# Kernel tuning notes

Measured on AMD Instinct MI355X. Metric: run time of the kernel, lower is better.

Reference implementation:

```python
import jax, jax.numpy as jnp
import numpy as np

B, S, E, H = 8, 2048, 1024, 4
D = E // H  # per-head attention embed_dim (torch MHA with num_heads=1)


def setup_inputs() -> dict:
    key = jax.random.key(0)
    ks = jax.random.split(key, 7)
    scale = 0.02
    return {
        "x": jax.random.normal(ks[0], (B, S, E), dtype=jnp.float32),
        # outer linear: torch Linear(E, E) -> y = x @ W.T + b
        "W_lin": jax.random.normal(ks[1], (E, E), dtype=jnp.float32) * scale,
        "b_lin": jnp.zeros((E,), dtype=jnp.float32),
        # per-head MultiheadAttention params, stacked over H heads
        # in_proj: [3D, D] weight, [3D] bias per head (q,k,v stacked)
        "W_in": jax.random.normal(ks[2], (H, 3 * D, D), dtype=jnp.float32) * scale,
        "b_in": jnp.zeros((H, 3 * D), dtype=jnp.float32),
        # out_proj: [D, D] weight, [D] bias per head
        "W_out": jax.random.normal(ks[3], (H, D, D), dtype=jnp.float32) * scale,
        "b_out": jnp.zeros((H, D), dtype=jnp.float32),
    }


def _forward(x, W_lin, b_lin, W_in, b_in, W_out, b_out):
    # outer projection
    x_proj = jnp.einsum("bse,fe->bsf", x, W_lin) + b_lin          # [B,S,E]
    # torch.chunk(dim=-1) into H contiguous slices of width D == reshape
    xs = x_proj.reshape(B, S, H, D)                                 # [B,S,H,D]
    # per-head in_proj (q,k,v share input; weights stacked as [3D, D])
    qkv = jnp.einsum("bshd,hed->bshe", xs, W_in) + b_in             # [B,S,H,3D]
    q, k, v = jnp.split(qkv, 3, axis=-1)                            # each [B,S,H,D]
    # scaled dot-product attention per head (inner num_heads=1 -> head dim D)
    scores = jnp.einsum("bshd,bthd->bhst", q, k) / jnp.sqrt(jnp.float32(D))
    attn = jax.nn.softmax(scores, axis=-1)                          # [B,H,S,S]
    out = jnp.einsum("bhst,bthd->bshd", attn, v)                    # [B,S,H,D]
    # per-head out_proj
    out = jnp.einsum("bshd,hed->bshe", out, W_out) + b_out          # [B,S,H,D]
    # concat heads back along feature dim
    return out.reshape(B, S, E)


def reference(x, W_lin, b_lin, W_in, b_in, W_out, b_out):
    return _forward(x, W_lin, b_lin, W_in, b_in, W_out, b_out)
```

## Files before the change

kernel.cpp:

```cpp
#include <hip/hip_runtime.h>


typedef unsigned short u16;
typedef short s8v __attribute__((ext_vector_type(8)));
typedef float f4v __attribute__((ext_vector_type(4)));
typedef unsigned short us8v __attribute__((ext_vector_type(8)));

typedef const __attribute__((address_space(1))) void* gas_t;
typedef __attribute__((address_space(3))) void* las_t;

#define QSCALE 0.09016844f

__device__ __forceinline__ u16 f2bf(float f) {
  unsigned u = __builtin_bit_cast(unsigned, f);
  unsigned r = u + 0x7FFFu + ((u >> 16) & 1u);
  return (u16)(r >> 16);
}

__device__ __forceinline__ unsigned cvtpk(float a, float b) {
  unsigned r;
  asm("v_cvt_pk_bf16_f32 %0, %1, %2" : "=v"(r) : "v"(a), "v"(b));
  return r;
}

__device__ __forceinline__ void gload16(const void* g, void* l) {
  __builtin_amdgcn_global_load_lds((gas_t)g, (las_t)l, 16, 0, 0);
}

__global__ void cast_kernel(const float* __restrict__ in, u16* __restrict__ out, int n4) {
  int i = blockIdx.x * blockDim.x + threadIdx.x;
  const int stride = gridDim.x * blockDim.x;
  for (; i < n4; i += stride) {
    const float4 v = reinterpret_cast<const float4*>(in)[i];
    ushort4 o;
    o.x = f2bf(v.x); o.y = f2bf(v.y); o.z = f2bf(v.z); o.w = f2bf(v.w);
    reinterpret_cast<ushort4*>(out)[i] = o;
  }
}

__global__ void cast_weights(const float* __restrict__ Wl, const float* __restrict__ Wi,
                             const float* __restrict__ Wo,
                             u16* __restrict__ WLb, u16* __restrict__ WIb,
                             u16* __restrict__ WOb) {
  const int i = blockIdx.x * blockDim.x + threadIdx.x;
  const float* src;
  u16* dst;
  int j;
  float sc = 1.0f;
  if (i < 262144) {
    src = Wl; dst = WLb; j = i;
  } else if (i < 458752) {
    src = Wi; dst = WIb; j = i - 262144;
    if (((j >> 6) % 768) < 256) sc = QSCALE;
  } else {
    src = Wo; dst = WOb; j = i - 458752;
  }
  const float4 v = reinterpret_cast<const float4*>(src)[j];
  ushort4 o;
  o.x = f2bf(v.x * sc); o.y = f2bf(v.y * sc); o.z = f2bf(v.z * sc); o.w = f2bf(v.w * sc);
  reinterpret_cast<ushort4*>(dst)[j] = o;
}

template <int MODE>
__global__ void __launch_bounds__(256, 2) gemm128(
    const u16* __restrict__ A, const u16* __restrict__ Bw,
    const float* __restrict__ bias,
    u16* __restrict__ outB, float* __restrict__ outF,
    u16* __restrict__ Qo, u16* __restrict__ Ko, u16* __restrict__ Vo)
{
  constexpr int K    = (MODE == 0) ? 1024 : 256;
  constexpr int LDA  = 1024;
  constexpr int LDB  = (MODE == 0) ? 1024 : 256;
  constexpr int SMEM = (MODE == 1) ? 35072 : 32768;

  const int bx = blockIdx.x, ny = blockIdx.y, h = blockIdx.z;
  const int tid = threadIdx.x;
  const int wid = tid >> 6, l = tid & 63;
  const int l15 = l & 15, lg = l >> 4;
  const int wr = wid >> 1, wc = wid & 1;

  __shared__ __align__(16) char smem[SMEM];
  char* Al = smem;
  char* Bl = smem + 16384;

  const u16* Abase = A + (size_t)bx * 128 * LDA + ((MODE == 0) ? 0 : h * 256);
  const size_t bwoff = (MODE == 0) ? 0
                      : ((MODE == 1) ? (size_t)h * 768 * 256 : (size_t)h * 256 * 256);
  const u16* Bbase = Bw + bwoff + (size_t)ny * 128 * LDB;

  f4v acc[4][4];
#pragma unroll
  for (int i = 0; i < 4; ++i)
#pragma unroll
    for (int j = 0; j < 4; ++j) acc[i][j] = f4v{0.f, 0.f, 0.f, 0.f};

  for (int k0 = 0; k0 < K; k0 += 64) {
    __syncthreads();
#pragma unroll
    for (int ii = 0; ii < 4; ++ii) {
      const int i = wid * 4 + ii;
      const int row = i * 8 + (l >> 3);
      const int c = l & 7;
      gload16(Abase + (size_t)row * LDA + k0 + ((c ^ (row & 7)) << 3), Al + i * 1024);
    }
#pragma unroll
    for (int ii = 0; ii < 4; ++ii) {
      const int i = wid * 4 + ii;
      const int row = i * 8 + (l >> 3);
      const int c = l & 7;
      gload16(Bbase + (size_t)row * LDB + k0 + ((c ^ (row & 7)) << 3), Bl + i * 1024);
    }
    __syncthreads();
#pragma unroll
    for (int kf = 0; kf < 2; ++kf) {
      s8v a[4];
#pragma unroll
      for (int mf = 0; mf < 4; ++mf) {
        const int row = wr * 64 + mf * 16 + l15;
        a[mf] = *reinterpret_cast<const s8v*>(
            Al + row * 128 + (((kf * 32 + lg * 8) << 1) ^ ((row & 7) << 4)));
      }
#pragma unroll
      for (int nf = 0; nf < 4; ++nf) {
        const int n = wc * 64 + nf * 16 + l15;
        const s8v b = *reinterpret_cast<const s8v*>(
            Bl + n * 128 + (((kf * 32 + lg * 8) << 1) ^ ((n & 7) << 4)));
#pragma unroll
        for (int mf = 0; mf < 4; ++mf)
          acc[mf][nf] = __builtin_amdgcn_mfma_f32_16x16x32_bf16(a[mf], b, acc[mf][nf], 0, 0, 0);
      }
    }
  }

  const int mbase = bx * 128 + wr * 64;
  const int nbase = ny * 128 + wc * 64;

  if constexpr (MODE == 0) {
#pragma unroll
    for (int nf = 0; nf < 4; ++nf) {
      const int colg = nbase + nf * 16 + l15;
      const float bv = bias[colg];
#pragma unroll
      for (int mf = 0; mf < 4; ++mf)
#pragma unroll
        for (int r = 0; r < 4; ++r) {
          const int mr = mbase + mf * 16 + lg * 4 + r;
          outB[(size_t)mr * 1024 + colg] = f2bf(acc[mf][nf][r] + bv);
        }
    }
  } else if constexpr (MODE == 2) {
#pragma unroll
    for (int nf = 0; nf < 4; ++nf) {
      const int colg = nbase + nf * 16 + l15;
      const float bv = bias[h * 256 + colg];
#pragma unroll
      for (int mf = 0; mf < 4; ++mf)
#pragma unroll
        for (int r = 0; r < 4; ++r) {
          const int mr = mbase + mf * 16 + lg * 4 + r;
          outF[(size_t)mr * 1024 + h * 256 + colg] = acc[mf][nf][r] + bv;
        }
    }
  } else {
    if (ny < 4) {
      u16* dst = (ny < 2) ? Qo : Ko;
      const int cb = (ny < 2) ? 0 : 256;
#pragma unroll
      for (int nf = 0; nf < 4; ++nf) {
        const int colg = nbase + nf * 16 + l15;
        const float bscale = (ny < 2) ? QSCALE : 1.0f;
        const float bv = bias[h * 768 + colg] * bscale;
        const int d = colg - cb;
#pragma unroll
        for (int mf = 0; mf < 4; ++mf)
#pragma unroll
          for (int r = 0; r < 4; ++r) {
            const int mr = mbase + mf * 16 + lg * 4 + r;
            const int b = mr >> 11, s = mr & 2047;
            dst[((size_t)(b * 4 + h) * 2048 + s) * 256 + d] = f2bf(acc[mf][nf][r] + bv);
          }
      }
    } else {
      __syncthreads();
      short* tr = reinterpret_cast<short*>(smem);
#pragma unroll
      for (int nf = 0; nf < 4; ++nf) {
        const int colg = nbase + nf * 16 + l15;
        const float bv = bias[h * 768 + colg];
        const int cl = wc * 64 + nf * 16 + l15;
#pragma unroll
        for (int mf = 0; mf < 4; ++mf)
#pragma unroll
          for (int r = 0; r < 4; ++r) {
            const int rl = wr * 64 + mf * 16 + lg * 4 + r;
            tr[rl * 137 + cl] = (short)f2bf(acc[mf][nf][r] + bv);
          }
      }
      __syncthreads();
      const int b = bx >> 4;
#pragma unroll
      for (int rep = 0; rep < 8; ++rep) {
        const int u = rep * 256 + tid;
        const int d = u >> 4, sb = u & 15;
        const int dglob = (ny - 4) * 128 + d;
        const int tile = (bx & 15) * 2 + (sb >> 3);
        const int c = sb & 7;
        const int kA = 32 * (c >> 2) + 8 * ((2 * c) & 3) + 4 * ((c >> 1) & 1);
        u16* base = Vo + (((size_t)(b * 4 + h) * 32 + tile) * 256 + dglob) * 64;
        ushort4 lo, hi;
        lo.x = (u16)tr[(sb * 8 + 0) * 137 + d];
        lo.y = (u16)tr[(sb * 8 + 1) * 137 + d];
        lo.z = (u16)tr[(sb * 8 + 2) * 137 + d];
        lo.w = (u16)tr[(sb * 8 + 3) * 137 + d];
        hi.x = (u16)tr[(sb * 8 + 4) * 137 + d];
        hi.y = (u16)tr[(sb * 8 + 5) * 137 + d];
        hi.z = (u16)tr[(sb * 8 + 6) * 137 + d];
        hi.w = (u16)tr[(sb * 8 + 7) * 137 + d];
        *reinterpret_cast<ushort4*>(base + kA)     = lo;
        *reinterpret_cast<ushort4*>(base + kA + 8) = hi;
      }
    }
  }
}

__global__ void __launch_bounds__(256, 2) attn_fwd(
    const u16* __restrict__ Q, const u16* __restrict__ Kk,
    const u16* __restrict__ Vt, u16* __restrict__ AO)
{
  const int qt = blockIdx.x;
  const int bh = blockIdx.y;
  const int tid = threadIdx.x;
  const int wid = tid >> 6, l = tid & 63;
  const int l15 = l & 15, lg = l >> 4;

  __shared__ __align__(16) char smem[65536];
  char* Kl = smem;
  char* Vl = smem + 32768;

  const size_t kbase = (size_t)bh * 2048 * 256;

  s8v qa[8];
  {
    const u16* qrow = Q + ((size_t)bh * 2048 + qt * 64 + wid * 16 + l15) * 256;
#pragma unroll
    for (int kf = 0; kf < 8; ++kf)
      qa[kf] = *reinterpret_cast<const s8v*>(qrow + kf * 32 + lg * 8);
  }

  f4v O[16];
#pragma unroll
  for (int df = 0; df < 16; ++df) O[df] = f4v{0.f, 0.f, 0.f, 0.f};
  float m_run = -1e30f, l_run = 0.f;

  for (int t0 = 0; t0 < 2048; t0 += 64) {
    __syncthreads();
#pragma unroll
    for (int ii = 0; ii < 8; ++ii) {
      const int i = wid * 8 + ii;
      const int row = i * 2 + (l >> 5);
      const int c = l & 31;
      gload16(Kk + kbase + (size_t)(t0 + row) * 256 + ((c ^ (row & 7)) << 3), Kl + i * 1024);
    }
    {
      const u16* vtile = Vt + ((size_t)bh * 32 + (t0 >> 6)) * 16384;
#pragma unroll
      for (int ii = 0; ii < 8; ++ii) {
        const int i = wid * 8 + ii;
        const int d = i * 8 + (l >> 3);
        const int c = l & 7;
        gload16(vtile + (size_t)d * 64 + ((c ^ (d & 7)) << 3), Vl + i * 1024);
      }
    }
    __syncthreads();

    f4v Sx[4];
#pragma unroll
    for (int nf = 0; nf < 4; ++nf) Sx[nf] = f4v{0.f, 0.f, 0.f, 0.f};
#pragma unroll
    for (int kf = 0; kf < 8; ++kf) {
      const int ch = kf * 4 + lg;
#pragma unroll
      for (int nf = 0; nf < 4; ++nf) {
        const int tl = nf * 16 + l15;
        const s8v kb = *reinterpret_cast<const s8v*>(
            Kl + tl * 512 + ((ch ^ (tl & 7)) << 4));
        Sx[nf] = __builtin_amdgcn_mfma_f32_16x16x32_bf16(kb, qa[kf], Sx[nf], 0, 0, 0);
      }
    }

    float mloc = fmaxf(fmaxf(fmaxf(Sx[0][0], Sx[0][1]), fmaxf(Sx[0][2], Sx[0][3])),
                       fmaxf(fmaxf(Sx[1][0], Sx[1][1]), fmaxf(Sx[1][2], Sx[1][3])));
    mloc = fmaxf(mloc, fmaxf(fmaxf(Sx[2][0], Sx[2][1]), fmaxf(Sx[2][2], Sx[2][3])));
    mloc = fmaxf(mloc, fmaxf(fmaxf(Sx[3][0], Sx[3][1]), fmaxf(Sx[3][2], Sx[3][3])));
    mloc = fmaxf(mloc, __shfl_xor(mloc, 16));
    mloc = fmaxf(mloc, __shfl_xor(mloc, 32));

    if (__any(mloc > m_run + 11.5f)) {
      const float mn = fmaxf(m_run, mloc);
      const float fac = __builtin_exp2f(m_run - mn);
      m_run = mn;
      l_run *= fac;
      float facr[4];
#pragma unroll
      for (int r = 0; r < 4; ++r) facr[r] = __shfl(fac, lg * 4 + r);
#pragma unroll
      for (int df = 0; df < 16; ++df) {
        O[df][0] *= facr[0]; O[df][1] *= facr[1];
        O[df][2] *= facr[2]; O[df][3] *= facr[3];
      }
    }

    float p[4][4];
    float sum = 0.f;
#pragma unroll
    for (int nf = 0; nf < 4; ++nf)
#pragma unroll
      for (int r = 0; r < 4; ++r) {
        p[nf][r] = __builtin_exp2f(Sx[nf][r] - m_run);
        sum += p[nf][r];
      }
    sum += __shfl_xor(sum, 16);
    sum += __shfl_xor(sum, 32);
    l_run += sum;

    s8v pa[2];
#pragma unroll
    for (int kf2 = 0; kf2 < 2; ++kf2) {
      int4 w;
      w.x = (int)cvtpk(p[2 * kf2][0],     p[2 * kf2][1]);
      w.y = (int)cvtpk(p[2 * kf2][2],     p[2 * kf2][3]);
      w.z = (int)cvtpk(p[2 * kf2 + 1][0], p[2 * kf2 + 1][1]);
      w.w = (int)cvtpk(p[2 * kf2 + 1][2], p[2 * kf2 + 1][3]);
      pa[kf2] = __builtin_bit_cast(s8v, w);
    }

#pragma unroll
    for (int kf2 = 0; kf2 < 2; ++kf2) {
      const int ch = kf2 * 4 + lg;
#pragma unroll
      for (int df = 0; df < 16; ++df) {
        const int dl = df * 16 + l15;
        const s8v vb = *reinterpret_cast<const s8v*>(
            Vl + dl * 128 + ((ch ^ (dl & 7)) << 4));
        O[df] = __builtin_amdgcn_mfma_f32_16x16x32_bf16(pa[kf2], vb, O[df], 0, 0, 0);
      }
    }
  }

  const float inv = 1.0f / l_run;
  float invr[4];
#pragma unroll
  for (int r = 0; r < 4; ++r) invr[r] = __shfl(inv, lg * 4 + r);
  const int b = bh >> 2, h = bh & 3;
#pragma unroll
  for (int df = 0; df < 16; ++df)
#pragma unroll
    for (int r = 0; r < 4; ++r) {
      const int srow = qt * 64 + wid * 16 + lg * 4 + r;
      AO[(size_t)(b * 2048 + srow) * 1024 + h * 256 + df * 16 + l15] =
          f2bf(O[df][r] * invr[r]);
    }
}

extern "C" void kernel_launch(void* const* d_in, const int* in_sizes, int n_in,
                              void* d_out, int out_size, void* d_ws, size_t ws_size,
                              hipStream_t stream) {
  (void)in_sizes; (void)n_in; (void)out_size; (void)ws_size;
  const float* x     = (const float*)d_in[0];
  const float* W_lin = (const float*)d_in[1];
  const float* b_lin = (const float*)d_in[2];
  const float* W_in  = (const float*)d_in[3];
  const float* b_in  = (const float*)d_in[4];
  const float* W_out = (const float*)d_in[5];
  const float* b_out = (const float*)d_in[6];

  char* ws = (char*)d_ws;
  u16* Qb  = (u16*)(ws);
  u16* Vtb = (u16*)(ws + (32ull << 20));
  u16* AOb = (u16*)(ws + (64ull << 20));
  u16* WLb = (u16*)(ws + (96ull << 20));
  u16* WIb = (u16*)(ws + (98ull << 20));
  u16* WOb = (u16*)(ws + (98ull << 20) + 1572864ull);

  char* doc  = (char*)d_out;
  u16* xb    = (u16*)doc;
  u16* xproj = (u16*)(doc + (32ull << 20));
  u16* Kb    = (u16*)doc;
  float* outF = (float*)d_out;

  cast_kernel<<<2048, 256, 0, stream>>>(x, xb, 4194304);
  cast_weights<<<2048, 256, 0, stream>>>(W_lin, W_in, W_out, WLb, WIb, WOb);

  gemm128<0><<<dim3(128, 8, 1), 256, 0, stream>>>(xb, WLb, b_lin, xproj, nullptr,
                                                  nullptr, nullptr, nullptr);
  gemm128<1><<<dim3(128, 6, 4), 256, 0, stream>>>(xproj, WIb, b_in, nullptr, nullptr,
                                                  Qb, Kb, Vtb);
  attn_fwd<<<dim3(32, 32, 1), 256, 0, stream>>>(Qb, Kb, Vtb, AOb);
  gemm128<2><<<dim3(128, 2, 4), 256, 0, stream>>>(AOb, WOb, b_out, nullptr, outF,
                                                  nullptr, nullptr, nullptr);
}
```

Before: 327.3 us.

## Fuse per-head output projection into attention kernel epilogue

The attention kernel now stages its normalized output tile in shared memory and multiplies it by the per-head W_out directly, adding the bias and writing fp32 output. This removes the separate out-projection GEMM launch and the bf16 round-trip of the attention output through global memory. K is moved to workspace so the fused kernel can write the output buffer while K is still being read. In exchange, W_out fragments are read straight from global/L2 by every block with no LDS reuse, and the epilogue adds register pressure to the attention kernel.

```diff
diff --git a/kernel.cpp b/kernel.cpp
--- a/kernel.cpp
+++ b/kernel.cpp
@@ -65,7 +65,7 @@
 __global__ void __launch_bounds__(256, 2) gemm128(
     const u16* __restrict__ A, const u16* __restrict__ Bw,
     const float* __restrict__ bias,
-    u16* __restrict__ outB, float* __restrict__ outF,
+    u16* __restrict__ outB,
     u16* __restrict__ Qo, u16* __restrict__ Ko, u16* __restrict__ Vo)
 {
   constexpr int K    = (MODE == 0) ? 1024 : 256;
@@ -84,8 +84,7 @@
   char* Bl = smem + 16384;
 
   const u16* Abase = A + (size_t)bx * 128 * LDA + ((MODE == 0) ? 0 : h * 256);
-  const size_t bwoff = (MODE == 0) ? 0
-                      : ((MODE == 1) ? (size_t)h * 768 * 256 : (size_t)h * 256 * 256);
+  const size_t bwoff = (MODE == 0) ? 0 : (size_t)h * 768 * 256;
   const u16* Bbase = Bw + bwoff + (size_t)ny * 128 * LDB;
 
   f4v acc[4][4];
@@ -146,19 +145,6 @@
         for (int r = 0; r < 4; ++r) {
           const int mr = mbase + mf * 16 + lg * 4 + r;
           outB[(size_t)mr * 1024 + colg] = f2bf(acc[mf][nf][r] + bv);
-        }
-    }
-  } else if constexpr (MODE == 2) {
-#pragma unroll
-    for (int nf = 0; nf < 4; ++nf) {
-      const int colg = nbase + nf * 16 + l15;
-      const float bv = bias[h * 256 + colg];
-#pragma unroll
-      for (int mf = 0; mf < 4; ++mf)
-#pragma unroll
-        for (int r = 0; r < 4; ++r) {
-          const int mr = mbase + mf * 16 + lg * 4 + r;
-          outF[(size_t)mr * 1024 + h * 256 + colg] = acc[mf][nf][r] + bv;
         }
     }
   } else {
@@ -225,7 +211,8 @@
 
 __global__ void __launch_bounds__(256, 2) attn_fwd(
     const u16* __restrict__ Q, const u16* __restrict__ Kk,
-    const u16* __restrict__ Vt, u16* __restrict__ AO)
+    const u16* __restrict__ Vt, const u16* __restrict__ Wout,
+    const float* __restrict__ bout, float* __restrict__ outF)
 {
   const int qt = blockIdx.x;
   const int bh = blockIdx.y;
@@ -347,19 +334,56 @@
     }
   }
 
-  const float inv = 1.0f / l_run;
-  float invr[4];
-#pragma unroll
-  for (int r = 0; r < 4; ++r) invr[r] = __shfl(inv, lg * 4 + r);
+  __syncthreads();
+
+  {
+    const float inv = 1.0f / l_run;
+    float invr[4];
+#pragma unroll
+    for (int r = 0; r < 4; ++r) invr[r] = __shfl(inv, lg * 4 + r);
+    char* Ol = smem + wid * 8192;
+#pragma unroll
+    for (int df = 0; df < 16; ++df)
+#pragma unroll
+      for (int r = 0; r < 4; ++r) {
+        const int row = lg * 4 + r;
+        const int byte = row * 512 + ((l15 & 7) << 1)
+                       + (((df * 2 + (l15 >> 3)) ^ (row & 7)) << 4);
+        *(short*)(Ol + byte) = (short)f2bf(O[df][r] * invr[r]);
+      }
+  }
+  asm volatile("s_waitcnt lgkmcnt(0)" ::: "memory");
+  __builtin_amdgcn_sched_barrier(0);
+
   const int b = bh >> 2, h = bh & 3;
-#pragma unroll
-  for (int df = 0; df < 16; ++df)
+  const u16* wb = Wout + (size_t)h * 256 * 256;
+
+  f4v acc[16];
+#pragma unroll
+  for (int eb = 0; eb < 16; ++eb) acc[eb] = f4v{0.f, 0.f, 0.f, 0.f};
+
+#pragma unroll
+  for (int ks = 0; ks < 8; ++ks) {
+    const s8v af = *reinterpret_cast<const s8v*>(
+        smem + wid * 8192 + l15 * 512 + (((ks * 4 + lg) ^ (l15 & 7)) << 4));
+#pragma unroll
+    for (int eb = 0; eb < 16; ++eb) {
+      const s8v wf = *reinterpret_cast<const s8v*>(
+          wb + (size_t)(eb * 16 + l15) * 256 + ks * 32 + lg * 8);
+      acc[eb] = __builtin_amdgcn_mfma_f32_16x16x32_bf16(af, wf, acc[eb], 0, 0, 0);
+    }
+  }
+
+#pragma unroll
+  for (int eb = 0; eb < 16; ++eb) {
+    const float bv = bout[h * 256 + eb * 16 + l15];
 #pragma unroll
     for (int r = 0; r < 4; ++r) {
       const int srow = qt * 64 + wid * 16 + lg * 4 + r;
-      AO[(size_t)(b * 2048 + srow) * 1024 + h * 256 + df * 16 + l15] =
-          f2bf(O[df][r] * invr[r]);
-    }
+      outF[(size_t)(b * 2048 + srow) * 1024 + h * 256 + eb * 16 + l15] =
+          acc[eb][r] + bv;
+    }
+  }
 }
 
 extern "C" void kernel_launch(void* const* d_in, const int* in_sizes, int n_in,
@@ -377,7 +401,7 @@
   char* ws = (char*)d_ws;
   u16* Qb  = (u16*)(ws);
   u16* Vtb = (u16*)(ws + (32ull << 20));
-  u16* AOb = (u16*)(ws + (64ull << 20));
+  u16* Kb  = (u16*)(ws + (64ull << 20));
   u16* WLb = (u16*)(ws + (96ull << 20));
   u16* WIb = (u16*)(ws + (98ull << 20));
   u16* WOb = (u16*)(ws + (98ull << 20) + 1572864ull);
@@ -385,17 +409,14 @@
   char* doc  = (char*)d_out;
   u16* xb    = (u16*)doc;
   u16* xproj = (u16*)(doc + (32ull << 20));
-  u16* Kb    = (u16*)doc;
   float* outF = (float*)d_out;
 
   cast_kernel<<<2048, 256, 0, stream>>>(x, xb, 4194304);
   cast_weights<<<2048, 256, 0, stream>>>(W_lin, W_in, W_out, WLb, WIb, WOb);
 
-  gemm128<0><<<dim3(128, 8, 1), 256, 0, stream>>>(xb, WLb, b_lin, xproj, nullptr,
+  gemm128<0><<<dim3(128, 8, 1), 256, 0, stream>>>(xb, WLb, b_lin, xproj,
                                                   nullptr, nullptr, nullptr);
-  gemm128<1><<<dim3(128, 6, 4), 256, 0, stream>>>(xproj, WIb, b_in, nullptr, nullptr,
+  gemm128<1><<<dim3(128, 6, 4), 256, 0, stream>>>(xproj, WIb, b_in, nullptr,
                                                   Qb, Kb, Vtb);
-  attn_fwd<<<dim3(32, 32, 1), 256, 0, stream>>>(Qb, Kb, Vtb, AOb);
-  gemm128<2><<<dim3(128, 2, 4), 256, 0, stream>>>(AOb, WOb, b_out, nullptr, outF,
-                                                  nullptr, nullptr, nullptr);
-}
+  attn_fwd<<<dim3(32, 32, 1), 256, 0, stream>>>(Qb, Kb, Vtb, WOb, b_out, outF);
+}
```

New measurement: 362.6 us. 10.8% more time.
